# Performance work log

Measured on AMD Instinct MI355X. Metric: run time of the kernel, lower is better.

## Reference

```python
import jax, jax.numpy as jnp
import numpy as np
import math

B, T, A, Z, E, H = 4, 16, 512, 512, 64, 8
HD = Z // H
NF = 6  # num Fourier freqs


def setup_inputs() -> dict:
    key = jax.random.key(0)
    ks = jax.random.split(key, 16)
    w = lambda k, shape: jax.random.normal(k, shape, jnp.float32) * 0.02
    return dict(
        z_current=jax.random.normal(ks[0], (B, A, Z), jnp.float32),
        z_pred=jax.random.normal(ks[1], (B, T, A, Z), jnp.float32),
        actions=jax.random.normal(ks[2], (B, T, 4), jnp.float32),
        Wq=w(ks[3], (Z, Z)), Wk=w(ks[4], (Z, Z)), Wv=w(ks[5], (Z, Z)),
        We=w(ks[6], (E, Z)), Wo=w(ks[7], (Z, Z)),
        g_lnq=jnp.ones((Z,), jnp.float32), b_lnq=jnp.zeros((Z,), jnp.float32),
        g_lno=jnp.ones((Z,), jnp.float32), b_lno=jnp.zeros((Z,), jnp.float32),
        W_ff1=w(ks[8], (Z, 4 * Z)), b_ff1=jnp.zeros((4 * Z,), jnp.float32),
        W_ff2=w(ks[9], (4 * Z, Z)), b_ff2=jnp.zeros((Z,), jnp.float32),
        W_edge=w(ks[10], (3 * 2 * NF + 2, E)), b_edge=jnp.zeros((E,), jnp.float32),
        Wg1=w(ks[11], (2 * Z, Z)), bg1=jnp.zeros((Z,), jnp.float32),
        Wg2=w(ks[12], (Z, 1)), bg2=jnp.zeros((1,), jnp.float32),
    )


def _ln(x, g, b, eps=1e-5):
    m = jnp.mean(x, -1, keepdims=True)
    v = jnp.var(x, -1, keepdims=True)
    return (x - m) * jax.lax.rsqrt(v + eps) * g + b


def _fourier(a3):
    # a3: [B,T,3] -> [B,T, 2 + 6*NF]
    dx, dy, th = a3[..., 0:1], a3[..., 1:2], a3[..., 2:3]
    feats = [jnp.sin(th), jnp.cos(th)]
    for k in range(NF):
        f = (2.0 ** k) * math.pi
        feats += [jnp.sin(f * dx), jnp.cos(f * dx),
                  jnp.sin(f * dy), jnp.cos(f * dy),
                  jnp.sin(f * th), jnp.cos(f * th)]
    return jnp.concatenate(feats, -1)


def reference(z_current, z_pred, actions, Wq, Wk, Wv, We, Wo,
              g_lnq, b_lnq, g_lno, b_lno, W_ff1, b_ff1, W_ff2, b_ff2,
              W_edge, b_edge, Wg1, bg1, Wg2, bg2):
    q = _ln(z_pred, g_lnq, b_lnq) @ Wq                      # [B,T,A,Z]
    kc = z_current @ Wk                                      # [B,A,Z]
    vc = z_current @ Wv                                      # [B,A,Z]
    e = (_fourier(actions[..., :3]) @ W_edge + b_edge) @ We  # [B,T,Z]
    k = kc[:, None, :, :] + e[:, :, None, :]                 # [B,T,A,Z] (edge-biased keys)

    qh = q.reshape(B, T, A, H, HD)
    kh = k.reshape(B, T, A, H, HD)
    vh = vc.reshape(B, A, H, HD)

    # Non-standard attention: outer product over head INDEX (i,j in [0,H)),
    # elementwise along head_dim d -> logits [B,T,A,HD,H,H]
    logits = jnp.einsum('btaid,btajd->btadij', qh, kh) / math.sqrt(HD)
    attn = jax.lax.stop_gradient(jax.nn.softmax(logits, axis=-1))  # torch @no_grad softmax
    out_h = jnp.einsum('btadij,bajd->btaid', attn, vh)       # [B,T,A,H,HD]
    out = out_h.reshape(B, T, A, Z) @ Wo

    gate_inp = jnp.concatenate([out, z_pred], -1)            # [B,T,A,2Z]
    g = jax.nn.sigmoid(
        jax.nn.gelu(gate_inp @ Wg1 + bg1, approximate=False) @ Wg2 + bg2)  # [B,T,A,1]

    z_mid = _ln(z_pred + g * out, g_lno, b_lno)
    return z_mid + (jax.nn.gelu(z_mid @ W_ff1 + b_ff1, approximate=False) @ W_ff2 + b_ff2)
```

## Files before the change

### kernel.cpp

```cpp
#include <hip/hip_runtime.h>
#include <hip/hip_bf16.h>
#include <math.h>


typedef __bf16 bf16x8 __attribute__((ext_vector_type(8)));
typedef float f32x4 __attribute__((ext_vector_type(4)));

#define ROWS 32768
#define ZDIM 512

__device__ __forceinline__ void gload16(const void* gptr, void* ldsptr) {
  __builtin_amdgcn_global_load_lds(
      (const __attribute__((address_space(1))) unsigned int*)gptr,
      (__attribute__((address_space(3))) unsigned int*)ldsptr, 16, 0, 0);
}

__device__ __forceinline__ float gelu_f(float x) {
  return 0.5f * x * (1.0f + erff(x * 0.70710678118654752f));
}

__global__ void transpose_f32_bf16(const float* __restrict__ in,
                                   __bf16* __restrict__ out, int R, int C) {
  __shared__ float tile[32][33];
  int c0 = blockIdx.x * 32, r0 = blockIdx.y * 32;
#pragma unroll
  for (int i = 0; i < 32; i += 8)
    tile[i + threadIdx.y][threadIdx.x] =
        in[(size_t)(r0 + i + threadIdx.y) * C + c0 + threadIdx.x];
  __syncthreads();
#pragma unroll
  for (int i = 0; i < 32; i += 8)
    out[(size_t)(c0 + i + threadIdx.y) * R + r0 + threadIdx.x] =
        (__bf16)tile[threadIdx.x][i + threadIdx.y];
}

__global__ void cvt_f32_bf16(const float* __restrict__ in,
                             __bf16* __restrict__ out) {
  int i = (blockIdx.x * 256 + threadIdx.x) * 4;
  float4 v = *(const float4*)(in + i);
  out[i + 0] = (__bf16)v.x;
  out[i + 1] = (__bf16)v.y;
  out[i + 2] = (__bf16)v.z;
  out[i + 3] = (__bf16)v.w;
}

template <bool GATED, bool EMIT_RAW>
__global__ __launch_bounds__(256) void ln_kernel(
    const float* __restrict__ xa, const __bf16* __restrict__ xb,
    const float* __restrict__ gate, const float* __restrict__ gamma,
    const float* __restrict__ beta, __bf16* __restrict__ out,
    __bf16* __restrict__ raw) {
  int row = blockIdx.x;
  int tid = threadIdx.x;
  int i0 = tid * 2;
  const float* ra = xa + (size_t)row * ZDIM;
  float x0 = ra[i0], x1 = ra[i0 + 1];
  if (EMIT_RAW) {
    raw[(size_t)row * ZDIM + i0] = (__bf16)x0;
    raw[(size_t)row * ZDIM + i0 + 1] = (__bf16)x1;
  }
  if (GATED) {
    float gv = gate[row];
    const __bf16* rb = xb + (size_t)row * ZDIM;
    x0 += gv * (float)rb[i0];
    x1 += gv * (float)rb[i0 + 1];
  }
  float s = x0 + x1, s2 = x0 * x0 + x1 * x1;
#pragma unroll
  for (int off = 32; off > 0; off >>= 1) {
    s += __shfl_down(s, off);
    s2 += __shfl_down(s2, off);
  }
  __shared__ float red[8];
  int wave = tid >> 6, lane = tid & 63;
  if (lane == 0) { red[wave] = s; red[4 + wave] = s2; }
  __syncthreads();
  float ts = red[0] + red[1] + red[2] + red[3];
  float ts2 = red[4] + red[5] + red[6] + red[7];
  float mean = ts * (1.0f / ZDIM);
  float var = ts2 * (1.0f / ZDIM) - mean * mean;
  float rstd = rsqrtf(var + 1e-5f);
  float y0 = (x0 - mean) * rstd * gamma[i0] + beta[i0];
  float y1 = (x1 - mean) * rstd * gamma[i0 + 1] + beta[i0 + 1];
  out[(size_t)row * ZDIM + i0] = (__bf16)y0;
  out[(size_t)row * ZDIM + i0 + 1] = (__bf16)y1;
}

__global__ void edge_kernel(const float* __restrict__ actions,
                            const float* __restrict__ W_edge,
                            const float* __restrict__ b_edge,
                            const float* __restrict__ We,
                            float* __restrict__ e) {
  int bt = blockIdx.x;
  int tid = threadIdx.x;
  float dx = actions[bt * 4 + 0];
  float dy = actions[bt * 4 + 1];
  float th = actions[bt * 4 + 2];
  float feats[38];
  feats[0] = sinf(th);
  feats[1] = cosf(th);
  int idx = 2;
  float f = 3.14159265358979323846f;
#pragma unroll
  for (int k = 0; k < 6; k++) {
    feats[idx++] = sinf(f * dx);
    feats[idx++] = cosf(f * dx);
    feats[idx++] = sinf(f * dy);
    feats[idx++] = cosf(f * dy);
    feats[idx++] = sinf(f * th);
    feats[idx++] = cosf(f * th);
    f *= 2.0f;
  }
  __shared__ float hid[64];
  float h = b_edge[tid];
  for (int ff = 0; ff < 38; ff++) h += feats[ff] * W_edge[ff * 64 + tid];
  hid[tid] = h;
  __syncthreads();
#pragma unroll
  for (int i = 0; i < 8; i++) {
    int z = i * 64 + tid;
    float sacc = 0.0f;
    for (int j = 0; j < 64; j++) sacc += hid[j] * We[j * ZDIM + z];
    e[(size_t)bt * ZDIM + z] = sacc;
  }
}

__global__ __launch_bounds__(256) void attn_kernel(
    const __bf16* __restrict__ q, const __bf16* __restrict__ kvc,
    const float* __restrict__ e, __bf16* __restrict__ attn_out) {
  int row = blockIdx.x * 4 + (threadIdx.x >> 6);
  int lane = threadIdx.x & 63;
  int a = row & 511;
  int bt = row >> 9;
  int b = bt >> 4;
  const __bf16* qr = q + (size_t)row * ZDIM;
  const __bf16* kr = kvc + ((size_t)b * 512 + a) * 1024;
  const __bf16* vr = kr + 512;
  const float* er = e + (size_t)bt * ZDIM;
  float kv[8], vv[8], qv[8];
#pragma unroll
  for (int j = 0; j < 8; j++) {
    kv[j] = (float)kr[j * 64 + lane] + er[j * 64 + lane];
    vv[j] = (float)vr[j * 64 + lane];
  }
#pragma unroll
  for (int i = 0; i < 8; i++) qv[i] = (float)qr[i * 64 + lane];
  const float scale = 0.125f;
#pragma unroll
  for (int i = 0; i < 8; i++) {
    float lg[8], m = -1e30f;
#pragma unroll
    for (int j = 0; j < 8; j++) {
      lg[j] = qv[i] * kv[j] * scale;
      m = fmaxf(m, lg[j]);
    }
    float ssum = 0.0f, o = 0.0f;
#pragma unroll
    for (int j = 0; j < 8; j++) {
      float p = __expf(lg[j] - m);
      ssum += p;
      o += p * vv[j];
    }
    attn_out[(size_t)row * ZDIM + i * 64 + lane] = (__bf16)(o / ssum);
  }
}

__global__ __launch_bounds__(256) void gate_kernel(
    const __bf16* __restrict__ hg, const float* __restrict__ Wg2,
    const float* __restrict__ bg2, float* __restrict__ g) {
  int row = blockIdx.x * 4 + (threadIdx.x >> 6);
  int lane = threadIdx.x & 63;
  float s = 0.0f;
#pragma unroll
  for (int i = 0; i < 8; i++) {
    int z = i * 64 + lane;
    s += (float)hg[(size_t)row * ZDIM + z] * Wg2[z];
  }
#pragma unroll
  for (int off = 32; off > 0; off >>= 1) s += __shfl_down(s, off);
  if (lane == 0) g[row] = 1.0f / (1.0f + expf(-(s + bg2[0])));
}

template <bool CONCAT, int EPI, typename OT>
__global__ __launch_bounds__(256) void gemm_kernel(
    const __bf16* __restrict__ A1, const __bf16* __restrict__ A2, int ksplit,
    int lda, const __bf16* __restrict__ Bt, const float* __restrict__ bias,
    const __bf16* __restrict__ resid, OT* __restrict__ C, int N, int K) {
  __shared__ __align__(16) __bf16 As[2][128 * 32];
  __shared__ __align__(16) __bf16 Bs[2][128 * 32];
  const int tid = threadIdx.x;
  const int wave = tid >> 6, lane = tid & 63;
  const int m0 = blockIdx.x * 128, n0 = blockIdx.y * 128;
  const int srow = lane >> 2;
  const int scol = (lane & 3) * 8;
  const int wm = (wave & 1) * 64, wn = (wave >> 1) * 64;
  const int fr = lane & 15, fq = lane >> 4;

  f32x4 acc[4][4] = {};

  auto stage = [&](int buf, int kt) {
    const __bf16* Ap;
    int ka;
    if (CONCAT) {
      if (kt < ksplit) { Ap = A1; ka = kt; }
      else             { Ap = A2; ka = kt - ksplit; }
    } else { Ap = A1; ka = kt; }
#pragma unroll
    for (int c = 0; c < 2; c++) {
      int r = 32 * wave + 16 * c + srow;
      gload16(Ap + (size_t)(m0 + r) * lda + ka + scol,
              &As[buf][(32 * wave + 16 * c) * 32]);
      gload16(Bt + (size_t)(n0 + r) * K + kt + scol,
              &Bs[buf][(32 * wave + 16 * c) * 32]);
    }
  };

  auto compute = [&](int buf) {
    bf16x8 af[4], bfr[4];
#pragma unroll
    for (int t = 0; t < 4; t++) {
      af[t] = *(const bf16x8*)&As[buf][(wm + t * 16 + fr) * 32 + fq * 8];
      bfr[t] = *(const bf16x8*)&Bs[buf][(wn + t * 16 + fr) * 32 + fq * 8];
    }
#pragma unroll
    for (int mt = 0; mt < 4; mt++)
#pragma unroll
      for (int nt = 0; nt < 4; nt++)
        acc[mt][nt] = __builtin_amdgcn_mfma_f32_16x16x32_bf16(
            af[mt], bfr[nt], acc[mt][nt], 0, 0, 0);
  };

  const int nk = K >> 5;
  stage(0, 0);
  __syncthreads();
  int cur = 0;
  for (int t = 0; t < nk - 1; ++t) {
    stage(cur ^ 1, (t + 1) << 5);
    compute(cur);
    __syncthreads();
    cur ^= 1;
  }
  compute(cur);

#pragma unroll
  for (int mt = 0; mt < 4; mt++) {
#pragma unroll
    for (int nt = 0; nt < 4; nt++) {
      int col = n0 + wn + nt * 16 + fr;
#pragma unroll
      for (int r = 0; r < 4; r++) {
        int row = m0 + wm + mt * 16 + fq * 4 + r;
        float v = acc[mt][nt][r];
        if (EPI == 1) { v = gelu_f(v + bias[col]); }
        else if (EPI == 2) {
          v += bias[col] + (float)resid[(size_t)row * N + col];
        }
        C[(size_t)row * N + col] = (OT)v;
      }
    }
  }
}

extern "C" void kernel_launch(void* const* d_in, const int* in_sizes, int n_in,
                              void* d_out, int out_size, void* d_ws,
                              size_t ws_size, hipStream_t stream) {
  const float* z_current = (const float*)d_in[0];
  const float* z_pred = (const float*)d_in[1];
  const float* actions = (const float*)d_in[2];
  const float* Wq = (const float*)d_in[3];
  const float* Wk = (const float*)d_in[4];
  const float* Wv = (const float*)d_in[5];
  const float* We = (const float*)d_in[6];
  const float* Wo = (const float*)d_in[7];
  const float* g_lnq = (const float*)d_in[8];
  const float* b_lnq = (const float*)d_in[9];
  const float* g_lno = (const float*)d_in[10];
  const float* b_lno = (const float*)d_in[11];
  const float* W_ff1 = (const float*)d_in[12];
  const float* b_ff1 = (const float*)d_in[13];
  const float* W_ff2 = (const float*)d_in[14];
  const float* b_ff2 = (const float*)d_in[15];
  const float* W_edge = (const float*)d_in[16];
  const float* b_edge = (const float*)d_in[17];
  const float* Wg1 = (const float*)d_in[18];
  const float* bg1 = (const float*)d_in[19];
  const float* Wg2 = (const float*)d_in[20];
  const float* bg2 = (const float*)d_in[21];

  char* ws = (char*)d_ws;
  size_t off = 0;
  auto alloc = [&](size_t bytes) {
    void* p = ws + off;
    off += (bytes + 255) & ~(size_t)255;
    return p;
  };
  __bf16* WTkv = (__bf16*)alloc(1024 * 512 * 2);
  __bf16* WTq = (__bf16*)alloc(512 * 512 * 2);
  __bf16* WTo = (__bf16*)alloc(512 * 512 * 2);
  __bf16* WTg1 = (__bf16*)alloc(512 * 1024 * 2);
  __bf16* WTf1 = (__bf16*)alloc(2048 * 512 * 2);
  __bf16* WTf2 = (__bf16*)alloc(512 * 2048 * 2);
  __bf16* zc_bf = (__bf16*)alloc(2048 * 512 * 2);
  __bf16* zp_bf = (__bf16*)alloc((size_t)ROWS * ZDIM * 2);
  __bf16* kvc = (__bf16*)alloc(2048 * 1024 * 2);
  float* ebuf = (float*)alloc(64 * 512 * 4);
  float* gbuf = (float*)alloc(32768 * 4);
  __bf16* BUF_A = (__bf16*)alloc((size_t)2 * ROWS * ZDIM * 2);
  __bf16* BUF_B = BUF_A + (size_t)ROWS * ZDIM;
  __bf16* BUF_C = (__bf16*)alloc((size_t)ROWS * ZDIM * 2);
  (void)ws_size; (void)in_sizes; (void)n_in; (void)out_size;

  dim3 tb(32, 8);
  transpose_f32_bf16<<<dim3(16, 16), tb, 0, stream>>>(Wk, WTkv, 512, 512);
  transpose_f32_bf16<<<dim3(16, 16), tb, 0, stream>>>(Wv, WTkv + 512 * 512,
                                                      512, 512);
  transpose_f32_bf16<<<dim3(16, 16), tb, 0, stream>>>(Wq, WTq, 512, 512);
  transpose_f32_bf16<<<dim3(16, 16), tb, 0, stream>>>(Wo, WTo, 512, 512);
  transpose_f32_bf16<<<dim3(16, 32), tb, 0, stream>>>(Wg1, WTg1, 1024, 512);
  transpose_f32_bf16<<<dim3(64, 16), tb, 0, stream>>>(W_ff1, WTf1, 512, 2048);
  transpose_f32_bf16<<<dim3(16, 64), tb, 0, stream>>>(W_ff2, WTf2, 2048, 512);

  cvt_f32_bf16<<<1024, 256, 0, stream>>>(z_current, zc_bf);
  ln_kernel<false, true><<<ROWS, 256, 0, stream>>>(z_pred, nullptr, nullptr,
                                                   g_lnq, b_lnq, BUF_A, zp_bf);
  edge_kernel<<<64, 64, 0, stream>>>(actions, W_edge, b_edge, We, ebuf);
  gemm_kernel<false, 0, __bf16><<<dim3(16, 8), 256, 0, stream>>>(
      zc_bf, nullptr, 0, 512, WTkv, nullptr, nullptr, kvc, 1024, 512);
  gemm_kernel<false, 0, __bf16><<<dim3(256, 4), 256, 0, stream>>>(
      BUF_A, nullptr, 0, 512, WTq, nullptr, nullptr, BUF_B, 512, 512);
  attn_kernel<<<ROWS / 4, 256, 0, stream>>>(BUF_B, kvc, ebuf, BUF_A);
  gemm_kernel<false, 0, __bf16><<<dim3(256, 4), 256, 0, stream>>>(
      BUF_A, nullptr, 0, 512, WTo, nullptr, nullptr, BUF_B, 512, 512);
  gemm_kernel<true, 1, __bf16><<<dim3(256, 4), 256, 0, stream>>>(
      BUF_B, zp_bf, 512, 512, WTg1, bg1, nullptr, BUF_C, 512, 1024);
  gate_kernel<<<ROWS / 4, 256, 0, stream>>>(BUF_C, Wg2, bg2, gbuf);
  ln_kernel<true, false><<<ROWS, 256, 0, stream>>>(z_pred, BUF_B, gbuf, g_lno,
                                                   b_lno, BUF_C, nullptr);
  float* outp = (float*)d_out;
  __bf16* h1 = BUF_A;
  for (int c = 0; c < 2; c++) {
    const __bf16* zmid_c = BUF_C + (size_t)c * 16384 * 512;
    gemm_kernel<false, 1, __bf16><<<dim3(128, 16), 256, 0, stream>>>(
        zmid_c, nullptr, 0, 512, WTf1, b_ff1, nullptr, h1, 2048, 512);
    gemm_kernel<false, 2, float><<<dim3(128, 4), 256, 0, stream>>>(
        h1, nullptr, 0, 2048, WTf2, b_ff2, zmid_c,
        outp + (size_t)c * 16384 * 512, 512, 2048);
  }
}
```

Baseline: 680.5 us.

## Triple-buffer GEMM LDS staging with explicit vmcnt waits and setprio

Changes the GEMM main loop from double to triple buffering, issuing global->LDS loads three K-tiles ahead. Explicit s_waitcnt vmcnt counts and raw s_barrier replace __syncthreads, so only the oldest tile must have arrived before compute. Fragments are read into registers before the next stage overwrites the buffer, and s_setprio raises priority during the MFMA block. This adds LDS use (48KB), which may lower occupancy, and hard-coded vmcnt values depend on exactly 4 loads per stage.

Measured after the change: 629.7 us. -7.5%, faster.

```diff
diff --git a/kernel.cpp b/kernel.cpp
--- a/kernel.cpp
+++ b/kernel.cpp
@@ -186,8 +186,8 @@
     const __bf16* __restrict__ A1, const __bf16* __restrict__ A2, int ksplit,
     int lda, const __bf16* __restrict__ Bt, const float* __restrict__ bias,
     const __bf16* __restrict__ resid, OT* __restrict__ C, int N, int K) {
-  __shared__ __align__(16) __bf16 As[2][128 * 32];
-  __shared__ __align__(16) __bf16 Bs[2][128 * 32];
+  __shared__ __align__(16) __bf16 As[3][128 * 32];
+  __shared__ __align__(16) __bf16 Bs[3][128 * 32];
   const int tid = threadIdx.x;
   const int wave = tid >> 6, lane = tid & 63;
   const int m0 = blockIdx.x * 128, n0 = blockIdx.y * 128;
@@ -215,32 +215,41 @@
     }
   };
 
-  auto compute = [&](int buf) {
+  const int nk = K >> 5;
+  stage(0, 0);
+  stage(1, 32);
+  stage(2, 64);
+  int buf = 0;
+  for (int t = 0; t < nk; ++t) {
+    const int remain = nk - 1 - t;
+    if (remain >= 2)      asm volatile("s_waitcnt vmcnt(8)" ::: "memory");
+    else if (remain == 1) asm volatile("s_waitcnt vmcnt(4)" ::: "memory");
+    else                  asm volatile("s_waitcnt vmcnt(0)" ::: "memory");
+    __builtin_amdgcn_s_barrier();
+
     bf16x8 af[4], bfr[4];
 #pragma unroll
-    for (int t = 0; t < 4; t++) {
-      af[t] = *(const bf16x8*)&As[buf][(wm + t * 16 + fr) * 32 + fq * 8];
-      bfr[t] = *(const bf16x8*)&Bs[buf][(wn + t * 16 + fr) * 32 + fq * 8];
-    }
+    for (int x = 0; x < 4; x++) {
+      af[x] = *(const bf16x8*)&As[buf][(wm + x * 16 + fr) * 32 + fq * 8];
+      bfr[x] = *(const bf16x8*)&Bs[buf][(wn + x * 16 + fr) * 32 + fq * 8];
+    }
+    asm volatile("s_waitcnt lgkmcnt(0)" ::: "memory");
+    __builtin_amdgcn_sched_barrier(0);
+    __builtin_amdgcn_s_barrier();
+
+    if (t + 3 < nk) stage(buf, (t + 3) << 5);
+
+    __builtin_amdgcn_s_setprio(1);
 #pragma unroll
     for (int mt = 0; mt < 4; mt++)
 #pragma unroll
       for (int nt = 0; nt < 4; nt++)
         acc[mt][nt] = __builtin_amdgcn_mfma_f32_16x16x32_bf16(
             af[mt], bfr[nt], acc[mt][nt], 0, 0, 0);
-  };
-
-  const int nk = K >> 5;
-  stage(0, 0);
-  __syncthreads();
-  int cur = 0;
-  for (int t = 0; t < nk - 1; ++t) {
-    stage(cur ^ 1, (t + 1) << 5);
-    compute(cur);
-    __syncthreads();
-    cur ^= 1;
-  }
-  compute(cur);
+    __builtin_amdgcn_s_setprio(0);
+
+    buf = (buf == 2) ? 0 : buf + 1;
+  }
 
 #pragma unroll
   for (int mt = 0; mt < 4; mt++) {
```
